# Performance work log

Hardware: AMD Instinct MI355X
Metric: run time of the kernel (lower is better)

Reference implementation:

```python
import jax, jax.numpy as jnp
import numpy as np

B, L, D_MODEL = 2, 1024, 512
N_LAYERS = 4
D_INNER = 2 * D_MODEL          # expand=2
D_STATE = 16
D_CONV = 4
DT_RANK = D_MODEL // 16        # ceil(512/16)=32
EPS = 1e-5


def layernorm(x, w, b):
    m = jnp.mean(x, axis=-1, keepdims=True)
    v = jnp.var(x, axis=-1, keepdims=True)
    return (x - m) * jax.lax.rsqrt(v + EPS) * w + b


def selective_scan(u, delta, A, Bm, Cm, Dp):
    # u, delta: [b,l,d]; Bm, Cm: [b,l,n]; A: [d,n]; Dp: [d]
    def step(h, inp):
        dt_t, b_t, c_t, u_t = inp            # [b,d],[b,n],[b,n],[b,d]
        dA = jnp.exp(dt_t[:, :, None] * A)   # [b,d,n]
        h = dA * h + (dt_t * u_t)[:, :, None] * b_t[:, None, :]
        y = jnp.einsum('bdn,bn->bd', h, c_t)
        return h, y

    b, l, d = u.shape
    n = A.shape[1]
    h0 = jnp.zeros((b, d, n), u.dtype)
    xs = (jnp.swapaxes(delta, 0, 1), jnp.swapaxes(Bm, 0, 1),
          jnp.swapaxes(Cm, 0, 1), jnp.swapaxes(u, 0, 1))
    _, ys = jax.lax.scan(step, h0, xs)       # ys: [l,b,d]
    return jnp.swapaxes(ys, 0, 1) + u * Dp


def mamba(x, in_w, conv_w, conv_b, xp_w, dtp_w, dtp_b, A_log, Dp, out_w):
    # x: [b,l,D_MODEL]
    xz = x @ in_w.T                          # [b,l,2*d_inner]
    xc, z = jnp.split(xz, 2, axis=-1)
    xc = jnp.swapaxes(xc, 1, 2)              # [b,d_inner,l]
    xc = jax.lax.conv_general_dilated(
        xc, conv_w[:, None, :], (1,), [(D_CONV - 1, 0)],
        feature_group_count=D_INNER,
        dimension_numbers=('NCH', 'OIH', 'NCH')) + conv_b[None, :, None]
    xc = jax.nn.silu(jnp.swapaxes(xc, 1, 2))  # [b,l,d_inner]
    x_dbl = xc @ xp_w.T                       # [b,l,dt_rank+2n]
    dt = x_dbl[..., :DT_RANK]
    Bm = x_dbl[..., DT_RANK:DT_RANK + D_STATE]
    Cm = x_dbl[..., DT_RANK + D_STATE:]
    dt = jax.nn.softplus(dt @ dtp_w.T + dtp_b)
    A = -jnp.exp(A_log)
    y = selective_scan(xc, dt, A, Bm, Cm, Dp)
    y = y * jax.nn.silu(z)
    return y @ out_w.T


def forward(x, in_proj_w, conv_w, conv_b, x_proj_w, dt_proj_w, dt_proj_b,
            A_log, D_param, out_proj_w, ln_w, ln_b, fnorm_w, fnorm_b):
    residual = None
    for i in range(in_proj_w.shape[0]):
        residual = x if residual is None else x + residual
        xn = layernorm(x, ln_w[i], ln_b[i])  # norm of incoming x (as in torch src)
        h1 = mamba(xn, in_proj_w[i, 0], conv_w[i, 0], conv_b[i, 0],
                   x_proj_w[i, 0], dt_proj_w[i, 0], dt_proj_b[i, 0],
                   A_log[i, 0], D_param[i, 0], out_proj_w[i, 0])
        h2 = mamba(jnp.flip(xn, axis=1), in_proj_w[i, 1], conv_w[i, 1],
                   conv_b[i, 1], x_proj_w[i, 1], dt_proj_w[i, 1],
                   dt_proj_b[i, 1], A_log[i, 1], D_param[i, 1],
                   out_proj_w[i, 1])
        x = h1 + h2                           # bi_add: NOT flipped back, faithful
    x = x + residual
    return layernorm(x, fnorm_w, fnorm_b)


def setup_inputs() -> dict:
    key = jax.random.key(0)
    ks = jax.random.split(key, 8)
    P2 = (N_LAYERS, 2)
    inp = {}
    inp['x'] = jax.random.normal(ks[0], (B, L, D_MODEL), jnp.float32)
    inp['in_proj_w'] = jax.random.normal(ks[1], P2 + (2 * D_INNER, D_MODEL), jnp.float32) * 0.02
    inp['conv_w'] = jax.random.normal(ks[2], P2 + (D_INNER, D_CONV), jnp.float32) * 0.1
    inp['conv_b'] = jnp.zeros(P2 + (D_INNER,), jnp.float32)
    inp['x_proj_w'] = jax.random.normal(ks[3], P2 + (DT_RANK + 2 * D_STATE, D_INNER), jnp.float32) * 0.02
    inp['dt_proj_w'] = jax.random.normal(ks[4], P2 + (D_INNER, DT_RANK), jnp.float32) * (DT_RANK ** -0.5)
    inp['dt_proj_b'] = jnp.full(P2 + (D_INNER,), float(np.log(np.expm1(0.01))), jnp.float32)
    inp['A_log'] = jnp.broadcast_to(jnp.log(jnp.arange(1, D_STATE + 1, dtype=jnp.float32)), P2 + (D_INNER, D_STATE)).copy()
    inp['D_param'] = jnp.ones(P2 + (D_INNER,), jnp.float32)
    inp['out_proj_w'] = jax.random.normal(ks[5], P2 + (D_MODEL, D_INNER), jnp.float32) * 0.02
    inp['ln_w'] = jnp.ones((N_LAYERS, D_MODEL), jnp.float32)
    inp['ln_b'] = jnp.zeros((N_LAYERS, D_MODEL), jnp.float32)
    inp['fnorm_w'] = jnp.ones((D_MODEL,), jnp.float32)
    inp['fnorm_b'] = jnp.zeros((D_MODEL,), jnp.float32)
    return inp


def reference(x, in_proj_w, conv_w, conv_b, x_proj_w, dt_proj_w, dt_proj_b,
              A_log, D_param, out_proj_w, ln_w, ln_b, fnorm_w, fnorm_b):
    return forward(x, in_proj_w, conv_w, conv_b, x_proj_w, dt_proj_w,
                   dt_proj_b, A_log, D_param, out_proj_w, ln_w, ln_b,
                   fnorm_w, fnorm_b)
```

## Files before the change

kernel.cpp:

```cpp
#include <hip/hip_runtime.h>
#include <hip/hip_bf16.h>
#include <type_traits>

#define B_   2
#define L_   1024
#define DM   512
#define DI   1024
#define DS   16
#define DTR  32
#define ROWS (B_*L_)
#define NCH  32
#define CHUNK (L_/NCH)

#define PO_CW    0
#define PO_CB    32768
#define PO_XPW   40960
#define PO_DTW   565248
#define PO_DTB   827392
#define PO_ALOG  835584
#define PO_DP    966656
#define PO_LNW   974848
#define PO_LNB   976896
#define PO_FNW   978944
#define PO_FNB   979456
#define PO_END   979968

#define N_WIN    (4*2097152)
#define N_WOUT   (4*1048576)
#define N_X      1048576

typedef __bf16 bf16x8 __attribute__((ext_vector_type(8)));
typedef float  f32x4  __attribute__((ext_vector_type(4)));
using bf16 = __hip_bfloat16;

__device__ __forceinline__ bf16x8 ld8(const bf16* p){
    return *reinterpret_cast<const bf16x8*>(p);
}
__device__ __forceinline__ float b2f(bf16 v){ return __bfloat162float(v); }

__device__ __forceinline__ unsigned pkbf2(float a, float b){
    bf16 ha = __float2bfloat16(a), hb = __float2bfloat16(b);
    unsigned short ua = *(unsigned short*)&ha, ub = *(unsigned short*)&hb;
    return (unsigned)ua | ((unsigned)ub << 16);
}
__device__ __forceinline__ float unpk_lo(unsigned v){
    unsigned x = v << 16; return __builtin_bit_cast(float, x);
}
__device__ __forceinline__ float unpk_hi(unsigned v){
    unsigned x = v & 0xffff0000u; return __builtin_bit_cast(float, x);
}

__device__ __forceinline__ void async_cp16(const void* g, void* s){
    __builtin_amdgcn_global_load_lds(
        (const __attribute__((address_space(1))) unsigned int*)g,
        (__attribute__((address_space(3))) unsigned int*)s, 16, 0, 0);
}

__global__ void detect_kernel(const void* Dp_raw, int* flag){
    *flag = (*(const unsigned int*)Dp_raw == 0x3F800000u) ? 1 : 0;
}

__device__ __forceinline__ uint4 cv8(const void* s, long o, int f){
    union { bf16 h[8]; uint4 u; } v;
    if (f){
        const float* p = (const float*)s + o;
        float4 a = *(const float4*)p;
        float4 b = *(const float4*)(p+4);
        v.h[0]=__float2bfloat16(a.x); v.h[1]=__float2bfloat16(a.y);
        v.h[2]=__float2bfloat16(a.z); v.h[3]=__float2bfloat16(a.w);
        v.h[4]=__float2bfloat16(b.x); v.h[5]=__float2bfloat16(b.y);
        v.h[6]=__float2bfloat16(b.z); v.h[7]=__float2bfloat16(b.w);
    } else {
        v.u = *(const uint4*)((const bf16*)s + o);
    }
    return v.u;
}

__global__ void megacvt_kernel(const void* cw, const void* cb, const void* xpw,
                               const void* dtw, const void* dtb, const void* al,
                               const void* dp, const void* lnw, const void* lnb,
                               const void* fnw, const void* fnb,
                               const void* inw, const void* outw, const void* xin,
                               bf16* PP, bf16* WIN, bf16* WOUT,
                               float* X, float* R, const int* flag){
    long i = ((long)blockIdx.x*256 + threadIdx.x) * 8;
    int f = *flag;
    if (i < PO_END){
        const void* s; long o;
        if      (i < PO_CB)   { s = cw;  o = i; }
        else if (i < PO_XPW)  { s = cb;  o = i - PO_CB; }
        else if (i < PO_DTW)  { s = xpw; o = i - PO_XPW; }
        else if (i < PO_DTB)  { s = dtw; o = i - PO_DTW; }
        else if (i < PO_ALOG) { s = dtb; o = i - PO_DTB; }
        else if (i < PO_DP)   { s = al;  o = i - PO_ALOG; }
        else if (i < PO_LNW)  { s = dp;  o = i - PO_DP; }
        else if (i < PO_LNB)  { s = lnw; o = i - PO_LNW; }
        else if (i < PO_FNW)  { s = lnb; o = i - PO_LNB; }
        else if (i < PO_FNB)  { s = fnw; o = i - PO_FNW; }
        else                  { s = fnb; o = i - PO_FNB; }
        *(uint4*)&PP[i] = cv8(s, o, f);
        return;
    }
    i -= PO_END;
    if (i < N_WIN){ *(uint4*)&WIN[i] = cv8(inw, i, f); return; }
    i -= N_WIN;
    if (i < N_WOUT){
        long l = i >> 20, r = i & 1048575;
        long n = r >> 11, dir = (r >> 10) & 1, d = r & 1023;
        *(uint4*)&WOUT[i] = cv8(outw, ((l*2 + dir)*512 + n)*1024 + d, f);
        return;
    }
    i -= N_WOUT;
    if (i < N_X){
        float xv[8];
        if (f){
            *(float4*)&xv[0] = *(const float4*)((const float*)xin + i);
            *(float4*)&xv[4] = *(const float4*)((const float*)xin + i + 4);
        } else {
            union { uint4 u; bf16 h[8]; } w;
            w.u = *(const uint4*)((const bf16*)xin + i);
            #pragma unroll
            for (int j=0;j<8;++j) xv[j] = b2f(w.h[j]);
        }
        *(float4*)(X+i)   = make_float4(xv[0],xv[1],xv[2],xv[3]);
        *(float4*)(X+i+4) = make_float4(xv[4],xv[5],xv[6],xv[7]);
        float4 z = make_float4(0.f,0.f,0.f,0.f);
        *(float4*)(R+i)   = z;
        *(float4*)(R+i+4) = z;
    }
}

__global__ void ln_kernel(const float* __restrict__ P, int nparts,
                          float* __restrict__ R,
                          const bf16* __restrict__ w, const bf16* __restrict__ b,
                          void* __restrict__ out, int mode, const int* flag){
    int row = blockIdx.x, lane = threadIdx.x;
    size_t base = (size_t)row*DM + lane*8;
    float v[8];
    *(float4*)&v[0] = *(const float4*)(P+base);
    *(float4*)&v[4] = *(const float4*)(P+base+4);
    for (int k=1; k<nparts; ++k){
        float4 a0 = *(const float4*)(P + (size_t)k*1048576 + base);
        float4 a1 = *(const float4*)(P + (size_t)k*1048576 + base + 4);
        v[0]+=a0.x; v[1]+=a0.y; v[2]+=a0.z; v[3]+=a0.w;
        v[4]+=a1.x; v[5]+=a1.y; v[6]+=a1.z; v[7]+=a1.w;
    }
    if (mode == 0){
        float4 r0 = *(const float4*)(R+base);
        float4 r1 = *(const float4*)(R+base+4);
        r0.x += v[0]; r0.y += v[1]; r0.z += v[2]; r0.w += v[3];
        r1.x += v[4]; r1.y += v[5]; r1.z += v[6]; r1.w += v[7];
        *(float4*)(R+base)   = r0;
        *(float4*)(R+base+4) = r1;
    } else {
        float4 r0 = *(const float4*)(R+base);
        float4 r1 = *(const float4*)(R+base+4);
        v[0]+=r0.x; v[1]+=r0.y; v[2]+=r0.z; v[3]+=r0.w;
        v[4]+=r1.x; v[5]+=r1.y; v[6]+=r1.z; v[7]+=r1.w;
    }
    float s=0.f, sq=0.f;
    #pragma unroll
    for (int j=0;j<8;++j){ s += v[j]; sq += v[j]*v[j]; }
    #pragma unroll
    for (int off=32; off>=1; off>>=1){
        s  += __shfl_xor(s,  off, 64);
        sq += __shfl_xor(sq, off, 64);
    }
    float mean = s*(1.f/DM);
    float var  = sq*(1.f/DM) - mean*mean;
    float rs   = rsqrtf(var + 1e-5f);
    bf16x8 wv = ld8(w + lane*8), bv = ld8(b + lane*8);
    float res[8];
    #pragma unroll
    for (int j=0;j<8;++j)
        res[j] = (v[j]-mean)*rs*(float)wv[j] + (float)bv[j];
    if (mode == 1 && *flag){
        float* of = (float*)out;
        *(float4*)(of+base)   = make_float4(res[0],res[1],res[2],res[3]);
        *(float4*)(of+base+4) = make_float4(res[4],res[5],res[6],res[7]);
    } else {
        union { bf16 h[8]; uint4 u; } o;
        #pragma unroll
        for (int j=0;j<8;++j) o.h[j] = __float2bfloat16(res[j]);
        *(uint4*)((bf16*)out + base) = o.u;
    }
}

template<int WM, int WN, int SK, int BK, typename CT>
__global__ __launch_bounds__(WM*WN*64)
void gemm_lds(const bf16* __restrict__ A, const bf16* __restrict__ W,
              CT* __restrict__ C, int K, int lda, int ldw, int ldc,
              int selTiles, long wSel){
    constexpr int BM = WM*64, BN = WN*64, T = WM*WN*64;
    constexpr int KC = BK/8;
    constexpr int RA = (BM*KC)/T, RB = (BN*KC)/T;
    __shared__ __align__(16) bf16 sA[BM*BK];
    __shared__ __align__(16) bf16 sB[BN*BK];
    int tid = threadIdx.x;
    int mtile = blockIdx.y, ntile = blockIdx.x;
    if (mtile >= selTiles) W += wSel;
    int m0 = mtile*BM, n0 = ntile*BN;
    int kPer = K/SK, kBeg = blockIdx.z*kPer, kEnd = kBeg + kPer;
    if (SK > 1)
        C += (size_t)blockIdx.z * (size_t)(gridDim.y*BM) * (size_t)(gridDim.x*BN);
    int wave = tid>>6, lane = tid&63, quad = lane>>4, r = lane&15;
    int wrow = wave / WN, wcol = wave % WN;
    const bf16* Abase = A + (size_t)m0*lda;
    const bf16* Wbase = W + (size_t)n0*ldw;
    f32x4 acc[4][4] = {};
    for (int k0 = kBeg; k0 < kEnd; k0 += BK){
        #pragma unroll
        for (int rr=0; rr<RA; ++rr){
            int q = rr*T + tid;
            int row = q/KC, cp = q%KC;
            async_cp16(Abase + (size_t)row*lda + k0 + cp*8, &sA[q*8]);
        }
        #pragma unroll
        for (int rr=0; rr<RB; ++rr){
            int q = rr*T + tid;
            int row = q/KC, cp = q%KC;
            async_cp16(Wbase + (size_t)row*ldw + k0 + cp*8, &sB[q*8]);
        }
        __syncthreads();
        #pragma unroll
        for (int ko=0; ko<BK; ko+=32){
            bf16x8 af[4], bw[4];
            #pragma unroll
            for (int mt=0; mt<4; ++mt)
                af[mt] = *(const bf16x8*)&sA[(wrow*64 + mt*16 + r)*BK + ko + quad*8];
            #pragma unroll
            for (int nt=0; nt<4; ++nt)
                bw[nt] = *(const bf16x8*)&sB[(wcol*64 + nt*16 + r)*BK + ko + quad*8];
            #pragma unroll
            for (int mt=0; mt<4; ++mt)
                #pragma unroll
                for (int nt=0; nt<4; ++nt)
                    acc[mt][nt] = __builtin_amdgcn_mfma_f32_16x16x32_bf16(
                        af[mt], bw[nt], acc[mt][nt], 0,0,0);
        }
        __syncthreads();
    }
    #pragma unroll
    for (int mt=0; mt<4; ++mt){
        #pragma unroll
        for (int nt=0; nt<4; ++nt){
            int col = n0 + wcol*64 + nt*16 + r;
            #pragma unroll
            for (int ri=0; ri<4; ++ri){
                int row = m0 + wrow*64 + mt*16 + quad*4 + ri;
                size_t idx = (size_t)row*ldc + col;
                if constexpr (std::is_same<CT, bf16>::value)
                    C[idx] = __float2bfloat16(acc[mt][nt][ri]);
                else
                    C[idx] = acc[mt][nt][ri];
            }
        }
    }
}

__global__ void conv_kernel(const bf16* __restrict__ XZ, const bf16* __restrict__ cw,
                            const bf16* __restrict__ cb, const bf16* __restrict__ Dp,
                            bf16* __restrict__ XC, unsigned* __restrict__ GU){
    int id  = blockIdx.x*256 + threadIdx.x;
    int d   = (id & 511) * 2;
    int t   = (id >> 9) & (L_-1);
    int b   = (id >> 19) & 1;
    int dir = id >> 20;
    bf16x8 wv8 = ld8(cw + ((size_t)dir*DI + d)*4);
    unsigned pcb = *(const unsigned*)&cb[dir*DI + d];
    float acc0 = unpk_lo(pcb), acc1 = unpk_hi(pcb);
    #pragma unroll
    for (int k=0;k<4;++k){
        int tau = t - 3 + k;
        if (tau >= 0){
            int sig = dir ? (L_-1-tau) : tau;
            unsigned pz = *(const unsigned*)&XZ[((size_t)(b*L_ + sig))*4096 + dir*2048 + d];
            acc0 += (float)wv8[k]   * unpk_lo(pz);
            acc1 += (float)wv8[4+k] * unpk_hi(pz);
        }
    }
    float u0 = acc0 * (1.f/(1.f + __expf(-acc0)));
    float u1 = acc1 * (1.f/(1.f + __expf(-acc1)));
    size_t idx = ((size_t)dir*ROWS + (size_t)b*L_ + t)*DI + d;
    *(unsigned*)&XC[idx] = pkbf2(u0, u1);
    int sig3 = dir ? (L_-1-t) : t;
    unsigned pzz = *(const unsigned*)&XZ[((size_t)(b*L_ + sig3))*4096 + dir*2048 + 1024 + d];
    float z0 = unpk_lo(pzz), z1 = unpk_hi(pzz);
    float g0 = z0*(1.f/(1.f + __expf(-z0)));
    float g1 = z1*(1.f/(1.f + __expf(-z1)));
    unsigned pdv = *(const unsigned*)&Dp[dir*DI + d];
    *(uint2*)&GU[idx] = make_uint2(pkbf2(g0, u0*unpk_lo(pdv)*g0),
                                   pkbf2(g1, u1*unpk_hi(pdv)*g1));
}

__global__ void dtproj_kernel(const float* __restrict__ PX, const bf16* __restrict__ dtw,
                              const bf16* __restrict__ dtb, const bf16* __restrict__ XC,
                              unsigned* __restrict__ DTW, float* __restrict__ XD){
    int id  = blockIdx.x*256 + threadIdx.x;
    int d   = id & (DI-1);
    int row = (id >> 10) & (ROWS-1);
    int dir = id >> 21;
    int tid = threadIdx.x;
    int grow = dir*2048 + row;
    __shared__ float sXR[32];
    if (tid < 32){
        float s = 0.f;
        #pragma unroll
        for (int k=0;k<8;++k) s += PX[(size_t)k*262144 + (size_t)grow*64 + tid];
        sXR[tid] = s;
    } else if (tid < 64 && ((id >> 8) & 3) == 0){
        int j = tid - 32;
        float s = 0.f;
        #pragma unroll
        for (int k=0;k<8;++k) s += PX[(size_t)k*262144 + (size_t)grow*64 + 32 + j];
        XD[(size_t)row*128 + dir*64 + 32 + j] = s;
    }
    __syncthreads();
    const bf16* wp = dtw + ((size_t)dir*DI + d)*DTR;
    float acc = b2f(dtb[dir*DI + d]);
    #pragma unroll
    for (int kk=0;kk<4;++kk){
        bf16x8 wv = ld8(wp + kk*8);
        #pragma unroll
        for (int j=0;j<8;++j) acc += sXR[kk*8+j]*(float)wv[j];
    }
    float sp = acc > 20.f ? acc : log1pf(__expf(acc));
    size_t idx = ((size_t)dir*ROWS + row)*DI + d;
    float u = b2f(XC[idx]);
    DTW[idx] = pkbf2(sp, sp*u);
}

__global__ void scan_mid(const float* __restrict__ SP, const float* __restrict__ SH,
                         float* __restrict__ H0){
    int id   = blockIdx.x*256 + threadIdx.x;
    int dirb = id >> 14;
    int rest = id & 16383;
    float h = 0.f;
    #pragma unroll
    for (int c=0; c<NCH; ++c){
        size_t o = ((size_t)(dirb*NCH + c) << 14) + rest;
        H0[o] = h;
        h = SP[o]*h + SH[o];
    }
}

template<int PHASE>
__global__ __launch_bounds__(256)
void scan_phase(const unsigned* __restrict__ DTW, const unsigned* __restrict__ GU,
                const float* __restrict__ XD, const bf16* __restrict__ Al,
                float* __restrict__ SP, float* __restrict__ SH,
                const float* __restrict__ H0, bf16* __restrict__ Y){
    int dirb = blockIdx.z, dir = dirb >> 1, b = dirb & 1;
    int c    = blockIdx.y;
    int d0   = blockIdx.x*128;
    int tid  = threadIdx.x;
    int dl   = tid >> 1, nh = tid & 1;
    int d    = d0 + dl;

    __shared__ __align__(16) unsigned sDTW[CHUNK*128];
    __shared__ __align__(16) float    sBC[CHUNK][32];
    __shared__ __align__(16) unsigned sGU[(PHASE==3)?CHUNK*128:4];

    const unsigned* DTWb = DTW + ((size_t)dir*ROWS + b*L_ + c*CHUNK)*DI + d0;
    #pragma unroll
    for (int it=0; it<4; ++it){
        int q = it*256 + tid;
        int t = q >> 5, c4 = q & 31;
        async_cp16(DTWb + (size_t)t*DI + c4*4, &sDTW[q*4]);
    }
    if (PHASE == 3){
        const unsigned* GUb = GU + ((size_t)dir*ROWS + b*L_ + c*CHUNK)*DI + d0;
        #pragma unroll
        for (int it=0; it<4; ++it){
            int q = it*256 + tid;
            int t = q >> 5, c4 = q & 31;
            async_cp16(GUb + (size_t)t*DI + c4*4, &sGU[q*4]);
        }
    }
    {
        int t = tid >> 3, j = tid & 7;
        async_cp16(XD + ((size_t)(b*L_) + c*CHUNK + t)*128 + dir*64 + 32 + j*4,
                   &sBC[t][j*4]);
    }

    float An[8];
    {
        const bf16* ap = Al + ((size_t)dir*DI + d)*DS + nh*8;
        bf16x8 av = ld8(ap);
        #pragma unroll
        for (int j=0;j<8;++j) An[j] = -__expf((float)av[j]);
    }

    float h[8], pr[8];
    size_t so = ((size_t)(dirb*NCH + c)*DI + d)*DS + nh*8;
    if (PHASE == 3){
        f32x4 h0a = *(const f32x4*)&H0[so];
        f32x4 h0b = *(const f32x4*)&H0[so+4];
        #pragma unroll
        for (int j=0;j<4;++j){ h[j] = h0a[j]; h[4+j] = h0b[j]; }
    } else {
        #pragma unroll
        for (int j=0;j<8;++j) h[j] = 0.f;
    }
    #pragma unroll
    for (int j=0;j<8;++j) pr[j] = 1.f;
    __syncthreads();

    bf16* Yp = Y + ((size_t)b*L_ + c*CHUNK)*2048 + dir*DI + d;

    #pragma unroll 4
    for (int tl=0; tl<CHUNK; ++tl){
        unsigned dw = sDTW[tl*128 + dl];
        float dtv = unpk_lo(dw), wv = unpk_hi(dw);
        f32x4 Bv0 = *(const f32x4*)&sBC[tl][nh*8];
        f32x4 Bv1 = *(const f32x4*)&sBC[tl][nh*8+4];
        f32x4 Cv0 = *(const f32x4*)&sBC[tl][16+nh*8];
        f32x4 Cv1 = *(const f32x4*)&sBC[tl][16+nh*8+4];
        float y = 0.f;
        #pragma unroll
        for (int j=0;j<4;++j){
            float dA0 = __expf(dtv*An[j]);
            float dA1 = __expf(dtv*An[4+j]);
            h[j]   = dA0*h[j]   + wv*Bv0[j];
            h[4+j] = dA1*h[4+j] + wv*Bv1[j];
            if (PHASE == 1){ pr[j] *= dA0; pr[4+j] *= dA1; }
            else { y += h[j]*Cv0[j]; y += h[4+j]*Cv1[j]; }
        }
        if (PHASE == 3){
            y += __shfl_xor(y, 1, 64);
            if (nh == 0){
                unsigned gu = sGU[tl*128 + dl];
                Yp[(size_t)tl*2048] = __float2bfloat16(y*unpk_lo(gu) + unpk_hi(gu));
            }
        }
    }
    if (PHASE == 1){
        *(f32x4*)&SP[so]   = *(f32x4*)&pr[0];
        *(f32x4*)&SP[so+4] = *(f32x4*)&pr[4];
        *(f32x4*)&SH[so]   = *(f32x4*)&h[0];
        *(f32x4*)&SH[so+4] = *(f32x4*)&h[4];
    }
}

extern "C" void kernel_launch(void* const* d_in, const int* in_sizes, int n_in,
                              void* d_out, int out_size, void* d_ws, size_t ws_size,
                              hipStream_t stream){
    const void* x_raw    = d_in[0];
    const void* inw_raw  = d_in[1];
    const void* convw_raw= d_in[2];
    const void* convb_raw= d_in[3];
    const void* xpw_raw  = d_in[4];
    const void* dtw_raw  = d_in[5];
    const void* dtb_raw  = d_in[6];
    const void* alog_raw = d_in[7];
    const void* dp_raw   = d_in[8];
    const void* outw_raw = d_in[9];
    const void* lnw_raw  = d_in[10];
    const void* lnb_raw  = d_in[11];
    const void* fnw_raw  = d_in[12];
    const void* fnb_raw  = d_in[13];

    char* ws = (char*)d_ws;
    float*    X   = (float*)   (ws + 0);
    float*    R   = (float*)   (ws + 4194304);
    bf16*     XN  = (bf16*)    (ws + 8388608);
    bf16*     XZ  = (bf16*)    (ws + 10485760);
    bf16*     XC  = (bf16*)    (ws + 27262976);
    float*    XD  = (float*)   (ws + 35651584);
    unsigned* DTW = (unsigned*)(ws + 36700160);
    unsigned* GU  = (unsigned*)(ws + 52428800);
    bf16*     Y   = (bf16*)    (ws + 68157440);
    float*    SP  = (float*)   (ws + 76546048);
    float*    SH  = (float*)   (ws + 84934656);
    bf16*     PP  = (bf16*)    (ws + 93323264);
    bf16*     WIN = (bf16*)    (ws + 95420416);
    bf16*     WOUT= (bf16*)    (ws + 112197632);
    float*    PX  = (float*)   (ws + 120586240);
    float*    PO  = (float*)   (ws + 128974848);
    int*      FLAG= (int*)     (ws + 145752064);
    float*    H0  = (float*)   (ws + 145752128);

    detect_kernel<<<1,1,0,stream>>>(dp_raw, FLAG);
    {
        long total = ((long)PO_END + N_WIN + N_WOUT + N_X) / 8;
        int blocks = (int)((total + 255)/256);
        megacvt_kernel<<<blocks,256,0,stream>>>(
            convw_raw, convb_raw, xpw_raw, dtw_raw, dtb_raw, alog_raw, dp_raw,
            lnw_raw, lnb_raw, fnw_raw, fnb_raw, inw_raw, outw_raw, x_raw,
            PP, WIN, WOUT, X, R, FLAG);
    }

    for (int l=0; l<4; ++l){
        ln_kernel<<<ROWS,64,0,stream>>>(l==0 ? X : PO, l==0 ? 1 : 4, R,
                                        PP+PO_LNW+l*DM, PP+PO_LNB+l*DM, XN, 0, FLAG);

        gemm_lds<2,2,1,64,bf16><<<dim3(32,16,1),256,0,stream>>>(
            XN, WIN + (size_t)l*2097152, XZ, 512, 512, 512, 4096, 1<<30, 0);

        conv_kernel<<<8192,256,0,stream>>>(XZ, PP+PO_CW + (size_t)l*2*DI*4,
                                           PP+PO_CB + l*2*DI, PP+PO_DP + l*2*DI,
                                           XC, GU);

        gemm_lds<2,1,8,64,float><<<dim3(1,32,8),128,0,stream>>>(
            XC, PP+PO_XPW + (size_t)l*2*64*DI, PX, 1024, 1024, 1024, 64,
            16, (long)64*DI);

        dtproj_kernel<<<16384,256,0,stream>>>(PX, PP+PO_DTW + (size_t)l*2*DI*DTR,
                                              PP+PO_DTB + l*2*DI, XC, DTW, XD);

        scan_phase<1><<<dim3(DI/128,NCH,4),256,0,stream>>>(
            DTW, GU, XD, PP+PO_ALOG + (size_t)l*2*DI*DS, SP, SH, H0, Y);
        scan_mid<<<256,256,0,stream>>>(SP, SH, H0);
        scan_phase<3><<<dim3(DI/128,NCH,4),256,0,stream>>>(
            DTW, GU, XD, PP+PO_ALOG + (size_t)l*2*DI*DS, SP, SH, H0, Y);

        gemm_lds<2,2,4,64,float><<<dim3(4,16,4),256,0,stream>>>(
            Y, WOUT + (size_t)l*1048576, PO, 2048, 2048, 2048, 512, 1<<30, 0);
    }

    ln_kernel<<<ROWS,64,0,stream>>>(PO, 4, R, PP+PO_FNW, PP+PO_FNB, d_out, 1, FLAG);
}
```

Baseline: 666.3 us.

## Fuse chunked scan phases into one persistent kernel with grid barriers

Merges the three scan launches (chunk-local pass, inter-chunk carry propagation, final output pass) into one kernel that uses software grid-wide barriers built on a global atomic counter. Each block keeps its DTW and GU tiles in LDS across phases, so they are not reloaded from global memory, and two kernel launches per layer are removed. It also folds log2(e) into A so the inner loop can call the native exp2. The cost is that all 1024 blocks must be co-resident (launch bounds set to 4 blocks per CU) or the spin barrier deadlocks, with a bounded retry as the only fallback; the extra shared memory for GU in the first phase may also lower occupancy.

```diff
diff --git a/kernel.cpp b/kernel.cpp
--- a/kernel.cpp
+++ b/kernel.cpp
@@ -11,6 +11,7 @@
 #define ROWS (B_*L_)
 #define NCH  32
 #define CHUNK (L_/NCH)
+#define NBLK 1024
 
 #define PO_CW    0
 #define PO_CB    32768
@@ -56,8 +57,23 @@
         (__attribute__((address_space(3))) unsigned int*)s, 16, 0, 0);
 }
 
-__global__ void detect_kernel(const void* Dp_raw, int* flag){
+__device__ __forceinline__ void grid_bar(unsigned* bar, unsigned target){
+    __threadfence();
+    __syncthreads();
+    if (threadIdx.x == 0){
+        atomicAdd(bar, 1u);
+        unsigned tries = 0;
+        while (__hip_atomic_load(bar, __ATOMIC_ACQUIRE, __HIP_MEMORY_SCOPE_AGENT) < target
+               && ++tries < (1u<<24))
+            __builtin_amdgcn_s_sleep(8);
+    }
+    __syncthreads();
+    __threadfence();
+}
+
+__global__ void detect_kernel(const void* Dp_raw, int* flag, unsigned* bar){
     *flag = (*(const unsigned int*)Dp_raw == 0x3F800000u) ? 1 : 0;
+    *bar  = 0u;
 }
 
 __device__ __forceinline__ uint4 cv8(const void* s, long o, int f){
@@ -330,26 +346,12 @@
     DTW[idx] = pkbf2(sp, sp*u);
 }
 
-__global__ void scan_mid(const float* __restrict__ SP, const float* __restrict__ SH,
-                         float* __restrict__ H0){
-    int id   = blockIdx.x*256 + threadIdx.x;
-    int dirb = id >> 14;
-    int rest = id & 16383;
-    float h = 0.f;
-    #pragma unroll
-    for (int c=0; c<NCH; ++c){
-        size_t o = ((size_t)(dirb*NCH + c) << 14) + rest;
-        H0[o] = h;
-        h = SP[o]*h + SH[o];
-    }
-}
-
-template<int PHASE>
-__global__ __launch_bounds__(256)
-void scan_phase(const unsigned* __restrict__ DTW, const unsigned* __restrict__ GU,
+__global__ __launch_bounds__(256, 4)
+void scan_fused(const unsigned* __restrict__ DTW, const unsigned* __restrict__ GU,
                 const float* __restrict__ XD, const bf16* __restrict__ Al,
                 float* __restrict__ SP, float* __restrict__ SH,
-                const float* __restrict__ H0, bf16* __restrict__ Y){
+                float* __restrict__ H0, bf16* __restrict__ Y,
+                unsigned* bar, unsigned genBase){
     int dirb = blockIdx.z, dir = dirb >> 1, b = dirb & 1;
     int c    = blockIdx.y;
     int d0   = blockIdx.x*128;
@@ -359,23 +361,16 @@
 
     __shared__ __align__(16) unsigned sDTW[CHUNK*128];
     __shared__ __align__(16) float    sBC[CHUNK][32];
-    __shared__ __align__(16) unsigned sGU[(PHASE==3)?CHUNK*128:4];
+    __shared__ __align__(16) unsigned sGU[CHUNK*128];
 
     const unsigned* DTWb = DTW + ((size_t)dir*ROWS + b*L_ + c*CHUNK)*DI + d0;
+    const unsigned* GUb  = GU  + ((size_t)dir*ROWS + b*L_ + c*CHUNK)*DI + d0;
     #pragma unroll
     for (int it=0; it<4; ++it){
         int q = it*256 + tid;
         int t = q >> 5, c4 = q & 31;
         async_cp16(DTWb + (size_t)t*DI + c4*4, &sDTW[q*4]);
-    }
-    if (PHASE == 3){
-        const unsigned* GUb = GU + ((size_t)dir*ROWS + b*L_ + c*CHUNK)*DI + d0;
-        #pragma unroll
-        for (int it=0; it<4; ++it){
-            int q = it*256 + tid;
-            int t = q >> 5, c4 = q & 31;
-            async_cp16(GUb + (size_t)t*DI + c4*4, &sGU[q*4]);
-        }
+        async_cp16(GUb  + (size_t)t*DI + c4*4, &sGU[q*4]);
     }
     {
         int t = tid >> 3, j = tid & 7;
@@ -388,26 +383,59 @@
         const bf16* ap = Al + ((size_t)dir*DI + d)*DS + nh*8;
         bf16x8 av = ld8(ap);
         #pragma unroll
-        for (int j=0;j<8;++j) An[j] = -__expf((float)av[j]);
+        for (int j=0;j<8;++j) An[j] = -__expf((float)av[j]) * 1.44269504f;
     }
 
     float h[8], pr[8];
+    #pragma unroll
+    for (int j=0;j<8;++j){ h[j]=0.f; pr[j]=1.f; }
+    __syncthreads();
+
+    #pragma unroll 4
+    for (int tl=0; tl<CHUNK; ++tl){
+        unsigned dw = sDTW[tl*128 + dl];
+        float dtv = unpk_lo(dw), wv = unpk_hi(dw);
+        f32x4 Bv0 = *(const f32x4*)&sBC[tl][nh*8];
+        f32x4 Bv1 = *(const f32x4*)&sBC[tl][nh*8+4];
+        #pragma unroll
+        for (int j=0;j<4;++j){
+            float dA0 = __builtin_amdgcn_exp2f(dtv*An[j]);
+            float dA1 = __builtin_amdgcn_exp2f(dtv*An[4+j]);
+            h[j]   = dA0*h[j]   + wv*Bv0[j];
+            h[4+j] = dA1*h[4+j] + wv*Bv1[j];
+            pr[j] *= dA0; pr[4+j] *= dA1;
+        }
+    }
     size_t so = ((size_t)(dirb*NCH + c)*DI + d)*DS + nh*8;
-    if (PHASE == 3){
+    *(f32x4*)&SP[so]   = *(f32x4*)&pr[0];
+    *(f32x4*)&SP[so+4] = *(f32x4*)&pr[4];
+    *(f32x4*)&SH[so]   = *(f32x4*)&h[0];
+    *(f32x4*)&SH[so+4] = *(f32x4*)&h[4];
+
+    grid_bar(bar, (genBase+1)*NBLK);
+
+    int gbid = blockIdx.x + gridDim.x*(blockIdx.y + gridDim.y*blockIdx.z);
+    if (gbid < 256){
+        int s = gbid*256 + tid;
+        int mdirb = s >> 14, rest = s & 16383;
+        float hh = 0.f;
+        #pragma unroll
+        for (int cc=0; cc<NCH; ++cc){
+            size_t o = ((size_t)(mdirb*NCH + cc) << 14) + rest;
+            H0[o] = hh;
+            hh = SP[o]*hh + SH[o];
+        }
+    }
+
+    grid_bar(bar, (genBase+2)*NBLK);
+
+    {
         f32x4 h0a = *(const f32x4*)&H0[so];
         f32x4 h0b = *(const f32x4*)&H0[so+4];
         #pragma unroll
         for (int j=0;j<4;++j){ h[j] = h0a[j]; h[4+j] = h0b[j]; }
-    } else {
-        #pragma unroll
-        for (int j=0;j<8;++j) h[j] = 0.f;
-    }
-    #pragma unroll
-    for (int j=0;j<8;++j) pr[j] = 1.f;
-    __syncthreads();
-
+    }
     bf16* Yp = Y + ((size_t)b*L_ + c*CHUNK)*2048 + dir*DI + d;
-
     #pragma unroll 4
     for (int tl=0; tl<CHUNK; ++tl){
         unsigned dw = sDTW[tl*128 + dl];
@@ -419,26 +447,18 @@
         float y = 0.f;
         #pragma unroll
         for (int j=0;j<4;++j){
-            float dA0 = __expf(dtv*An[j]);
-            float dA1 = __expf(dtv*An[4+j]);
+            float dA0 = __builtin_amdgcn_exp2f(dtv*An[j]);
+            float dA1 = __builtin_amdgcn_exp2f(dtv*An[4+j]);
             h[j]   = dA0*h[j]   + wv*Bv0[j];
             h[4+j] = dA1*h[4+j] + wv*Bv1[j];
-            if (PHASE == 1){ pr[j] *= dA0; pr[4+j] *= dA1; }
-            else { y += h[j]*Cv0[j]; y += h[4+j]*Cv1[j]; }
-        }
-        if (PHASE == 3){
-            y += __shfl_xor(y, 1, 64);
-            if (nh == 0){
-                unsigned gu = sGU[tl*128 + dl];
-                Yp[(size_t)tl*2048] = __float2bfloat16(y*unpk_lo(gu) + unpk_hi(gu));
-            }
-        }
-    }
-    if (PHASE == 1){
-        *(f32x4*)&SP[so]   = *(f32x4*)&pr[0];
-        *(f32x4*)&SP[so+4] = *(f32x4*)&pr[4];
-        *(f32x4*)&SH[so]   = *(f32x4*)&h[0];
-        *(f32x4*)&SH[so+4] = *(f32x4*)&h[4];
+            y += h[j]*Cv0[j];
+            y += h[4+j]*Cv1[j];
+        }
+        y += __shfl_xor(y, 1, 64);
+        if (nh == 0){
+            unsigned gu = sGU[tl*128 + dl];
+            Yp[(size_t)tl*2048] = __float2bfloat16(y*unpk_lo(gu) + unpk_hi(gu));
+        }
     }
 }
 
@@ -478,9 +498,10 @@
     float*    PX  = (float*)   (ws + 120586240);
     float*    PO  = (float*)   (ws + 128974848);
     int*      FLAG= (int*)     (ws + 145752064);
+    unsigned* BAR = (unsigned*)(ws + 145752068);
     float*    H0  = (float*)   (ws + 145752128);
 
-    detect_kernel<<<1,1,0,stream>>>(dp_raw, FLAG);
+    detect_kernel<<<1,1,0,stream>>>(dp_raw, FLAG, BAR);
     {
         long total = ((long)PO_END + N_WIN + N_WOUT + N_X) / 8;
         int blocks = (int)((total + 255)/256);
@@ -508,11 +529,9 @@
         dtproj_kernel<<<16384,256,0,stream>>>(PX, PP+PO_DTW + (size_t)l*2*DI*DTR,
                                               PP+PO_DTB + l*2*DI, XC, DTW, XD);
 
-        scan_phase<1><<<dim3(DI/128,NCH,4),256,0,stream>>>(
-            DTW, GU, XD, PP+PO_ALOG + (size_t)l*2*DI*DS, SP, SH, H0, Y);
-        scan_mid<<<256,256,0,stream>>>(SP, SH, H0);
-        scan_phase<3><<<dim3(DI/128,NCH,4),256,0,stream>>>(
-            DTW, GU, XD, PP+PO_ALOG + (size_t)l*2*DI*DS, SP, SH, H0, Y);
+        scan_fused<<<dim3(DI/128,NCH,4),256,0,stream>>>(
+            DTW, GU, XD, PP+PO_ALOG + (size_t)l*2*DI*DS,
+            SP, SH, H0, Y, BAR, (unsigned)(l*2));
 
         gemm_lds<2,2,4,64,float><<<dim3(4,16,4),256,0,stream>>>(
             Y, WOUT + (size_t)l*1048576, PO, 2048, 2048, 2048, 512, 1<<30, 0);
```

After: 2.631 ms. +294.9%, slower.
